# Kernel optimization log

Measured on AMD Instinct MI355X. Metric: run time of the kernel, lower is better.

The kernel has to match this reference:

```python
import jax, jax.numpy as jnp
import numpy as np


def setup_inputs() -> dict:
    key = jax.random.key(0)
    ks = jax.random.split(key, 6)
    B, T, D, E, F = 2, 2048, 1024, 8, 2048
    x = jax.random.normal(ks[0], (B, T, D), dtype=jnp.float32)
    gate_w = jax.random.normal(ks[1], (D, E), dtype=jnp.float32) * (1.0 / np.sqrt(D))
    base_w1 = jax.random.normal(ks[2], (D, F), dtype=jnp.float32) * np.sqrt(2.0 / (D + F))
    base_w2 = jax.random.normal(ks[3], (F, D), dtype=jnp.float32) * np.sqrt(2.0 / (F + D))
    expert_w1 = base_w1[None] + jax.random.normal(ks[4], (E, D, F), dtype=jnp.float32) * 0.01
    expert_w2 = base_w2[None] + jax.random.normal(ks[5], (E, F, D), dtype=jnp.float32) * 0.01
    expert_b1 = jnp.zeros((E, F), dtype=jnp.float32)
    expert_b2 = jnp.zeros((E, D), dtype=jnp.float32)
    return {"x": x, "gate_w": gate_w, "expert_w1": expert_w1, "expert_b1": expert_b1,
            "expert_w2": expert_w2, "expert_b2": expert_b2}


def reference(x, gate_w, expert_w1, expert_b1, expert_w2, expert_b2):
    # Router (TopKRouter): top-2 routing with aux load-balance loss + z-loss
    E = gate_w.shape[-1]
    TOP_K = 2
    Z_LOSS_COEF = 1e-3
    logits = jnp.einsum('btd,de->bte', x, gate_w)                       # [B,T,E]
    top_vals, top_idx = jax.lax.top_k(logits, TOP_K)                    # [B,T,K]
    router_weights = jax.nn.softmax(top_vals, axis=-1)                  # [B,T,K]
    probs = jax.nn.softmax(logits, axis=-1)
    mask = jax.nn.one_hot(top_idx[..., 0], E, dtype=x.dtype)            # top-1 expert mask
    tokens_per_expert = mask.mean(axis=(0, 1))                          # [E]
    router_prob_per_expert = probs.mean(axis=(0, 1))                    # [E]
    aux_loss = E * jnp.sum(tokens_per_expert * router_prob_per_expert) \
               + jnp.mean(logits ** 2) * Z_LOSS_COEF

    # Expert FFNs: compute all experts densely, then gather top-k outputs.
    # (Same math as per-token weight gather, without the BTDF intermediate.)
    h = jnp.einsum('btd,edf->btef', x, expert_w1) + expert_b1           # [B,T,E,F]
    h = jax.nn.gelu(h, approximate=False)                               # torch F.gelu default = erf
    out_all = jnp.einsum('btef,efd->bted', h, expert_w2) + expert_b2    # [B,T,E,D]
    gathered = jnp.take_along_axis(out_all, top_idx[..., None], axis=2) # [B,T,K,D]
    output = jnp.einsum('btk,btkd->btd', router_weights, gathered)      # [B,T,D]
    return output, aux_loss
```

## Files before the change

kernel.cpp:

```cpp
#include <hip/hip_runtime.h>
#include <hip/hip_bf16.h>

#define NTOK 4096
#define DDIM 1024
#define NEXP 8
#define FDIM 2048
#define CAP  4096
#define RTOK 16

typedef float f32x4 __attribute__((ext_vector_type(4)));
typedef short s16x8 __attribute__((ext_vector_type(8)));
typedef short s16x4 __attribute__((ext_vector_type(4)));

__device__ __forceinline__ unsigned short f2bf(float f) {
  unsigned int u = __float_as_uint(f);
  unsigned int r = u + 0x7fffu + ((u >> 16) & 1u);
  return (unsigned short)(r >> 16);
}

__device__ __forceinline__ void gload16(const void* g, void* l) {
  __builtin_amdgcn_global_load_lds(
      (__attribute__((address_space(1))) unsigned int*)(g),
      (__attribute__((address_space(3))) unsigned int*)(l), 16, 0, 0);
}

__global__ __launch_bounds__(256)
void k_transpose_cast(const float* __restrict__ src, unsigned short* __restrict__ dst,
                      int R, int C) {
  __shared__ float tile[64][68];
  const int e = blockIdx.z;
  const int c0 = blockIdx.x * 64, r0 = blockIdx.y * 64;
  const float* s = src + (size_t)e * R * C;
  unsigned short* d = dst + (size_t)e * R * C;
  const int tid = threadIdx.x;
  const int lr = tid >> 4, lc = (tid & 15) * 4;
  #pragma unroll
  for (int p = 0; p < 4; p++) {
    float4 v = *(const float4*)(s + (size_t)(r0 + p * 16 + lr) * C + c0 + lc);
    tile[p * 16 + lr][lc]     = v.x;
    tile[p * 16 + lr][lc + 1] = v.y;
    tile[p * 16 + lr][lc + 2] = v.z;
    tile[p * 16 + lr][lc + 3] = v.w;
  }
  __syncthreads();
  const int sc = tid >> 3, sr = (tid & 7) * 8;
  #pragma unroll
  for (int p = 0; p < 2; p++) {
    int c = p * 32 + sc;
    s16x8 o;
    #pragma unroll
    for (int j = 0; j < 8; j++) o[j] = (short)f2bf(tile[sr + j][c]);
    *(s16x8*)(d + (size_t)(c0 + c) * R + r0 + sr) = o;
  }
}

__global__ __launch_bounds__(128)
void k_router(const float* __restrict__ x, const float* __restrict__ gw,
              unsigned short* __restrict__ xb,
              float* __restrict__ topw, int* __restrict__ elist,
              int* __restrict__ ecnt, int* __restrict__ cnt1,
              float* __restrict__ psum, float* __restrict__ sqsum) {
  __shared__ float gwt[NEXP][DDIM + 4];
  __shared__ float xs[RTOK][264];
  __shared__ double lgd[RTOK][NEXP];
  __shared__ float bps[NEXP];
  __shared__ int bc[NEXP];
  __shared__ float bsq;
  const int tid = threadIdx.x;
  const int tok0 = blockIdx.x * RTOK;

  for (int i = tid; i < DDIM * NEXP; i += 128) {
    int d = i >> 3, e = i & 7;
    gwt[e][d] = gw[i];
  }
  if (tid < NEXP) { bps[tid] = 0.f; bc[tid] = 0; }
  if (tid == 0) bsq = 0.f;

  const int t = tid >> 3, e = tid & 7;
  double a0 = 0.0, a1 = 0.0, a2 = 0.0, a3 = 0.0;
  for (int c = 0; c < DDIM; c += 256) {
    __syncthreads();
    for (int i = tid; i < RTOK * 64; i += 128) {
      int r = i >> 6, c4 = i & 63;
      float4 v = *(const float4*)(x + (size_t)(tok0 + r) * DDIM + c + c4 * 4);
      *(float4*)&xs[r][c4 * 4] = v;
      s16x4 o;
      o[0] = (short)f2bf(v.x); o[1] = (short)f2bf(v.y);
      o[2] = (short)f2bf(v.z); o[3] = (short)f2bf(v.w);
      *(s16x4*)(xb + (size_t)(tok0 + r) * DDIM + c + c4 * 4) = o;
    }
    __syncthreads();
    #pragma unroll 8
    for (int d4 = 0; d4 < 64; d4++) {
      float4 xv = *(const float4*)&xs[t][d4 * 4];
      float4 gv = *(const float4*)&gwt[e][c + d4 * 4];
      a0 += (double)xv.x * (double)gv.x;
      a1 += (double)xv.y * (double)gv.y;
      a2 += (double)xv.z * (double)gv.z;
      a3 += (double)xv.w * (double)gv.w;
    }
  }
  lgd[t][e] = (a0 + a1) + (a2 + a3);
  __syncthreads();

  if (tid < RTOK) {
    int tok = tok0 + tid;
    double acc[NEXP];
    #pragma unroll
    for (int k = 0; k < NEXP; k++) acc[k] = lgd[tid][k];
    int i0 = 0; double v0 = acc[0];
    #pragma unroll
    for (int k = 1; k < NEXP; k++) if (acc[k] > v0) { v0 = acc[k]; i0 = k; }
    int i1 = (i0 == 0) ? 1 : 0; double v1 = acc[i1];
    #pragma unroll
    for (int k = 0; k < NEXP; k++) if (k != i0 && acc[k] > v1) { v1 = acc[k]; i1 = k; }
    float w0 = 1.0f / (1.0f + expf((float)(v1 - v0)));
    topw[2*tok] = w0; topw[2*tok + 1] = 1.0f - w0;
    int s0 = atomicAdd(&ecnt[i0], 1); elist[i0*CAP + s0] = 2*tok;
    int s1 = atomicAdd(&ecnt[i1], 1); elist[i1*CAP + s1] = 2*tok + 1;
    atomicAdd(&bc[i0], 1);
    float lm = (float)acc[0];
    #pragma unroll
    for (int k = 1; k < NEXP; k++) lm = fmaxf(lm, (float)acc[k]);
    float pe[NEXP], ps = 0.f, sq = 0.f;
    #pragma unroll
    for (int k = 0; k < NEXP; k++) {
      float le = (float)acc[k];
      pe[k] = expf(le - lm); ps += pe[k];
      sq += le * le;
    }
    float inv = 1.0f / ps;
    #pragma unroll
    for (int k = 0; k < NEXP; k++) atomicAdd(&bps[k], pe[k] * inv);
    atomicAdd(&bsq, sq);
  }
  __syncthreads();
  if (tid < NEXP) { atomicAdd(&psum[tid], bps[tid]); atomicAdd(&cnt1[tid], bc[tid]); }
  if (tid == 0) atomicAdd(sqsum, bsq);
}

template<int K, int N, bool GELU, bool ROWSHIFT>
__global__ __launch_bounds__(512)
void k_gemm(const unsigned short* __restrict__ A, const unsigned short* __restrict__ Bt,
            const float* __restrict__ bias, void* __restrict__ Out,
            const int* __restrict__ elist, const int* __restrict__ ecnt,
            const float* __restrict__ topw) {
  constexpr int BM = 128, BN = 128, BK = 128, WM = 2, WN = 4;
  constexpr int AISS = BM / 32;
  constexpr int BISS = BN / 32;
  constexpr int MF = BM / WM / 16;
  constexpr int NF = BN / WN / 16;
  __shared__ unsigned char lsA[BM * 256];
  __shared__ unsigned char lsB[BN * 256];
  const int e = blockIdx.z, mt = blockIdx.y, nt = blockIdx.x;
  const int cnt = ecnt[e];
  const int m0 = mt * BM;
  if (m0 >= cnt) return;
  const int rv = min(BM, cnt - m0);
  const int* lst = elist + e * CAP + m0;
  const int tid = threadIdx.x, wv = tid >> 6, lane = tid & 63;
  const int wm = wv / WN, wn = wv % WN;
  const unsigned short* Be = Bt + (size_t)e * N * K;

  const unsigned short* agp[AISS];
  const unsigned short* bgp[BISS];
  int adst[AISS], bdst[BISS];
  const int cu = tid & 15;
  #pragma unroll
  for (int li = 0; li < AISS; li++) {
    int r = li * 32 + (tid >> 4);
    int rr = (r < rv) ? r : 0;
    int aid = lst[rr];
    int arow = ROWSHIFT ? (aid >> 1) : aid;
    int csrc = (cu ^ (r & 15)) * 16;
    agp[li] = A + (size_t)arow * K + (csrc >> 1);
    adst[li] = r * 256 + cu * 16;
  }
  #pragma unroll
  for (int li = 0; li < BISS; li++) {
    int r = li * 32 + (tid >> 4);
    int csrc = (cu ^ (r & 15)) * 16;
    bgp[li] = Be + (size_t)(nt * BN + r) * K + (csrc >> 1);
    bdst[li] = r * 256 + cu * 16;
  }

  f32x4 acc[MF][NF];
  #pragma unroll
  for (int mi = 0; mi < MF; mi++)
    #pragma unroll
    for (int ni = 0; ni < NF; ni++)
      acc[mi][ni] = (f32x4){0.f, 0.f, 0.f, 0.f};

  constexpr int NK = K / BK;
  for (int t = 0; t < NK; ++t) {
    const int k0 = t * BK;
    #pragma unroll
    for (int li = 0; li < AISS; li++) gload16(agp[li] + k0, &lsA[adst[li]]);
    #pragma unroll
    for (int li = 0; li < BISS; li++) gload16(bgp[li] + k0, &lsB[bdst[li]]);
    __syncthreads();
    #pragma unroll
    for (int ks = 0; ks < 4; ks++) {
      s16x8 af[MF], bf[NF];
      #pragma unroll
      for (int mi = 0; mi < MF; mi++) {
        int row = wm * (BM / WM) + mi * 16 + (lane & 15);
        int c16 = (ks * 4 + (lane >> 4)) ^ (row & 15);
        af[mi] = *(const s16x8*)&lsA[row * 256 + c16 * 16];
      }
      #pragma unroll
      for (int ni = 0; ni < NF; ni++) {
        int row = wn * (BN / WN) + ni * 16 + (lane & 15);
        int c16 = (ks * 4 + (lane >> 4)) ^ (row & 15);
        bf[ni] = *(const s16x8*)&lsB[row * 256 + c16 * 16];
      }
      #pragma unroll
      for (int mi = 0; mi < MF; mi++)
        #pragma unroll
        for (int ni = 0; ni < NF; ni++)
          acc[mi][ni] = __builtin_amdgcn_mfma_f32_16x16x32_bf16(af[mi], bf[ni], acc[mi][ni], 0, 0, 0);
    }
    __syncthreads();
  }

  const int g4 = (lane >> 4) * 4, cn = lane & 15;
  #pragma unroll
  for (int mi = 0; mi < MF; mi++) {
    #pragma unroll
    for (int reg = 0; reg < 4; reg++) {
      int r = wm * (BM / WM) + mi * 16 + g4 + reg;
      if (r < rv) {
        int aid = lst[r];
        #pragma unroll
        for (int ni = 0; ni < NF; ni++) {
          int n = nt * BN + wn * (BN / WN) + ni * 16 + cn;
          float v = acc[mi][ni][reg] + bias[(size_t)e * N + n];
          if constexpr (GELU) {
            v = 0.5f * v * (1.0f + erff(v * 0.70710678118654752f));
            ((unsigned short*)Out)[(size_t)aid * N + n] = f2bf(v);
          } else {
            atomicAdd(&((float*)Out)[(size_t)(aid >> 1) * N + n], topw[aid] * v);
          }
        }
      }
    }
  }
}

__global__ void k_aux(const int* __restrict__ cnt1, const float* __restrict__ psum,
                      const float* __restrict__ sqsum, float* __restrict__ out) {
  if (threadIdx.x == 0 && blockIdx.x == 0) {
    float a = 0.f;
    for (int e = 0; e < NEXP; e++)
      a += ((float)cnt1[e] / (float)NTOK) * (psum[e] / (float)NTOK);
    out[(size_t)NTOK * DDIM] = (float)NEXP * a + (*sqsum) / (float)(NTOK * NEXP) * 1e-3f;
  }
}

extern "C" void kernel_launch(void* const* d_in, const int* in_sizes, int n_in,
                              void* d_out, int out_size, void* d_ws, size_t ws_size,
                              hipStream_t stream) {
  const float* x  = (const float*)d_in[0];
  const float* gw = (const float*)d_in[1];
  const float* w1 = (const float*)d_in[2];
  const float* b1 = (const float*)d_in[3];
  const float* w2 = (const float*)d_in[4];
  const float* b2 = (const float*)d_in[5];
  float* out = (float*)d_out;
  char* p = (char*)d_ws;

  int*   ecnt  = (int*)p;
  int*   cnt1  = (int*)(p + 32);
  float* psum  = (float*)(p + 64);
  float* sqsum = (float*)(p + 96);
  float* topw  = (float*)(p + 256);
  int*   elist = (int*)(p + 256 + 32768);
  unsigned short* xb  = (unsigned short*)(p + 256 + 32768 + 131072);
  unsigned short* w1t = xb  + (size_t)NTOK * DDIM;
  unsigned short* w2t = w1t + (size_t)NEXP * DDIM * FDIM;
  unsigned short* Hb  = w2t + (size_t)NEXP * DDIM * FDIM;

  hipMemsetAsync(p, 0, 128, stream);
  hipMemsetAsync(out, 0, (size_t)(NTOK * DDIM + 1) * 4, stream);
  k_transpose_cast<<<dim3(FDIM/64, DDIM/64, NEXP), 256, 0, stream>>>(w1, w1t, DDIM, FDIM);
  k_transpose_cast<<<dim3(DDIM/64, FDIM/64, NEXP), 256, 0, stream>>>(w2, w2t, FDIM, DDIM);
  k_router<<<NTOK / RTOK, 128, 0, stream>>>(x, gw, xb, topw, elist, ecnt, cnt1, psum, sqsum);
  k_gemm<DDIM, FDIM, true,  true ><<<dim3(FDIM/128, 16, NEXP), 512, 0, stream>>>(xb, w1t, b1, Hb, elist, ecnt, nullptr);
  k_gemm<FDIM, DDIM, false, false><<<dim3(DDIM/128, 16, NEXP), 512, 0, stream>>>(Hb, w2t, b2, out, elist, ecnt, topw);
  k_aux<<<1, 64, 0, stream>>>(cnt1, psum, sqsum, out);
}
```

Before: 277.5 us.

## Swizzle GEMM block order per XCD and replace atomic combine with separate pass

New measurement: 251.6 us. -9.3%, faster.

```diff
diff --git a/kernel.cpp b/kernel.cpp
--- a/kernel.cpp
+++ b/kernel.cpp
@@ -7,6 +7,7 @@
 #define FDIM 2048
 #define CAP  4096
 #define RTOK 16
+#define MT   16
 
 typedef float f32x4 __attribute__((ext_vector_type(4)));
 typedef short s16x8 __attribute__((ext_vector_type(8)));
@@ -143,16 +144,24 @@
 __global__ __launch_bounds__(512)
 void k_gemm(const unsigned short* __restrict__ A, const unsigned short* __restrict__ Bt,
             const float* __restrict__ bias, void* __restrict__ Out,
-            const int* __restrict__ elist, const int* __restrict__ ecnt,
-            const float* __restrict__ topw) {
+            const int* __restrict__ elist, const int* __restrict__ ecnt) {
   constexpr int BM = 128, BN = 128, BK = 128, WM = 2, WN = 4;
+  constexpr int GX = N / BN;
+  constexpr int TOT = GX * MT * NEXP;
+  constexpr int CHUNK = TOT / 8;
   constexpr int AISS = BM / 32;
   constexpr int BISS = BN / 32;
   constexpr int MF = BM / WM / 16;
   constexpr int NF = BN / WN / 16;
   __shared__ unsigned char lsA[BM * 256];
   __shared__ unsigned char lsB[BN * 256];
-  const int e = blockIdx.z, mt = blockIdx.y, nt = blockIdx.x;
+
+  const int w = blockIdx.x;
+  const int swz = (w & 7) * CHUNK + (w >> 3);
+  const int e = swz / (GX * MT);
+  const int loc = swz % (GX * MT);
+  const int mt = loc % MT, nt = loc / MT;
+
   const int cnt = ecnt[e];
   const int m0 = mt * BM;
   if (m0 >= cnt) return;
@@ -239,12 +248,25 @@
             v = 0.5f * v * (1.0f + erff(v * 0.70710678118654752f));
             ((unsigned short*)Out)[(size_t)aid * N + n] = f2bf(v);
           } else {
-            atomicAdd(&((float*)Out)[(size_t)(aid >> 1) * N + n], topw[aid] * v);
+            ((float*)Out)[(size_t)aid * N + n] = v;
           }
         }
       }
     }
   }
+}
+
+__global__ void k_combine(const float* __restrict__ buf, const float* __restrict__ topw,
+                          float* __restrict__ out) {
+  int i = blockIdx.x * 256 + threadIdx.x;
+  int t = i >> 8, c = i & 255;
+  float w0 = topw[2*t], w1 = topw[2*t + 1];
+  float4 a = ((const float4*)(buf + (size_t)(2*t) * DDIM))[c];
+  float4 b = ((const float4*)(buf + (size_t)(2*t + 1) * DDIM))[c];
+  float4 o;
+  o.x = w0*a.x + w1*b.x; o.y = w0*a.y + w1*b.y;
+  o.z = w0*a.z + w1*b.z; o.w = w0*a.w + w1*b.w;
+  ((float4*)out)[i] = o;
 }
 
 __global__ void k_aux(const int* __restrict__ cnt1, const float* __restrict__ psum,
@@ -279,13 +301,14 @@
   unsigned short* w1t = xb  + (size_t)NTOK * DDIM;
   unsigned short* w2t = w1t + (size_t)NEXP * DDIM * FDIM;
   unsigned short* Hb  = w2t + (size_t)NEXP * DDIM * FDIM;
+  float* obuf = (float*)(Hb + (size_t)NTOK * 2 * FDIM);
 
   hipMemsetAsync(p, 0, 128, stream);
-  hipMemsetAsync(out, 0, (size_t)(NTOK * DDIM + 1) * 4, stream);
   k_transpose_cast<<<dim3(FDIM/64, DDIM/64, NEXP), 256, 0, stream>>>(w1, w1t, DDIM, FDIM);
   k_transpose_cast<<<dim3(DDIM/64, FDIM/64, NEXP), 256, 0, stream>>>(w2, w2t, FDIM, DDIM);
   k_router<<<NTOK / RTOK, 128, 0, stream>>>(x, gw, xb, topw, elist, ecnt, cnt1, psum, sqsum);
-  k_gemm<DDIM, FDIM, true,  true ><<<dim3(FDIM/128, 16, NEXP), 512, 0, stream>>>(xb, w1t, b1, Hb, elist, ecnt, nullptr);
-  k_gemm<FDIM, DDIM, false, false><<<dim3(DDIM/128, 16, NEXP), 512, 0, stream>>>(Hb, w2t, b2, out, elist, ecnt, topw);
+  k_gemm<DDIM, FDIM, true,  true ><<<(FDIM/128)*MT*NEXP, 512, 0, stream>>>(xb, w1t, b1, Hb, elist, ecnt);
+  k_gemm<FDIM, DDIM, false, false><<<(DDIM/128)*MT*NEXP, 512, 0, stream>>>(Hb, w2t, b2, obuf, elist, ecnt);
+  k_combine<<<NTOK * DDIM / 4 / 256, 256, 0, stream>>>(obuf, topw, out);
   k_aux<<<1, 64, 0, stream>>>(cnt1, psum, sqsum, out);
 }
```
